# Optimization experiments

Hardware: AMD Instinct MI355X
Metric: run time of the kernel (lower is better)

The kernel has to match this reference:

```python
import jax, jax.numpy as jnp
import numpy as np

D_VOC, P_VOC, M_VOC = 2048, 1024, 4096
H = 256
T = 32
LD, LP, LM = 24, 12, 20


def _norm_adj(key, n):
    # binary graph + self loops, row-normalized (matches GCN.normalize(adj+I))
    a = (jax.random.uniform(key, (n, n)) < 0.002).astype(jnp.float32)
    a = a + jnp.eye(n, dtype=jnp.float32)
    rs = a.sum(axis=1)
    rinv = jnp.where(rs > 0, 1.0 / rs, 0.0)
    return rinv[:, None] * a


def setup_inputs() -> dict:
    key = jax.random.key(0)
    ks = jax.random.split(key, 32)
    s = float(1.0 / np.sqrt(H))
    u = lambda k, shape, sc: jax.random.uniform(k, shape, minval=-sc, maxval=sc, dtype=jnp.float32)
    inp = {
        'diag_codes': jax.random.randint(ks[0], (T, LD), 0, D_VOC),
        'proc_codes': jax.random.randint(ks[1], (T, LP), 0, P_VOC),
        'med_codes': jax.random.randint(ks[2], (T - 1, LM), 0, M_VOC),
        'diag_emb': u(ks[3], (D_VOC, H), 0.1),
        'proc_emb': u(ks[4], (P_VOC, H), 0.1),
        'gru_d_wih': u(ks[5], (3 * H, H), s), 'gru_d_whh': u(ks[6], (3 * H, H), s),
        'gru_d_bih': u(ks[7], (3 * H,), s), 'gru_d_bhh': u(ks[8], (3 * H,), s),
        'gru_p_wih': u(ks[9], (3 * H, H), s), 'gru_p_whh': u(ks[10], (3 * H, H), s),
        'gru_p_bih': u(ks[11], (3 * H,), s), 'gru_p_bhh': u(ks[12], (3 * H,), s),
        'q_w': u(ks[13], (2 * H, H), s), 'q_b': u(ks[14], (H,), s),
        'adj_ehr': _norm_adj(ks[15], M_VOC),
        'adj_ddi': _norm_adj(ks[16], M_VOC),
        'w1_ehr': u(ks[17], (M_VOC, H), s), 'b1_ehr': u(ks[18], (H,), s),
        'w2_ehr': u(ks[19], (H, H), s), 'b2_ehr': u(ks[20], (H,), s),
        'w1_ddi': u(ks[21], (M_VOC, H), s), 'b1_ddi': u(ks[22], (H,), s),
        'w2_ddi': u(ks[23], (H, H), s), 'b2_ddi': u(ks[24], (H,), s),
        'inter': jax.random.normal(ks[25], (1,), dtype=jnp.float32) / H,
        'proj_w': u(ks[26], (2 * H, H), s), 'proj_b': u(ks[27], (H,), s),
    }
    return inp


def _gru(x, wih, whh, bih, bhh):
    # torch.nn.GRU cell math; x: [T, H] -> outputs [T, H]
    def step(h, xt):
        gi = xt @ wih.T + bih
        gh = h @ whh.T + bhh
        ir, iz, inn = jnp.split(gi, 3)
        hr, hz, hn = jnp.split(gh, 3)
        r = jax.nn.sigmoid(ir + hr)
        z = jax.nn.sigmoid(iz + hz)
        n = jnp.tanh(inn + r * hn)
        h2 = (1.0 - z) * n + z * h
        return h2, h2
    _, ys = jax.lax.scan(step, jnp.zeros((x.shape[-1],), x.dtype), x)
    return ys


def _gcn(adj, w1, b1, w2, b2):
    # input features are identity, so first support mm(I, w1) == w1
    h1 = jax.nn.relu(adj @ w1 + b1)
    return adj @ (h1 @ w2) + b2


def reference(diag_codes, proc_codes, med_codes, diag_emb, proc_emb,
              gru_d_wih, gru_d_whh, gru_d_bih, gru_d_bhh,
              gru_p_wih, gru_p_whh, gru_p_bih, gru_p_bhh,
              q_w, q_b, adj_ehr, adj_ddi,
              w1_ehr, b1_ehr, w2_ehr, b2_ehr,
              w1_ddi, b1_ddi, w2_ddi, b2_ddi,
              inter, proj_w, proj_b):
    # ---- PatientEncoder: gather + sum codes per visit, GRU over visits ----
    seq_d = diag_emb[diag_codes].sum(axis=1)            # [T, H]
    seq_p = proc_emb[proc_codes].sum(axis=1)            # [T, H]
    od = _gru(seq_d, gru_d_wih, gru_d_whh, gru_d_bih, gru_d_bhh)
    op = _gru(seq_p, gru_p_wih, gru_p_whh, gru_p_bih, gru_p_bhh)
    feats = jnp.concatenate([od, op], axis=-1)          # [T, 2H]
    queries = jax.nn.relu(feats) @ q_w + q_b            # [T, H] (Sequential(ReLU, Linear))
    query = queries[-1:]                                # [1, H]
    history_keys = queries[:-1]                         # [T-1, H]
    # multi-hot history medication values (scatter)
    tm1 = med_codes.shape[0]
    history_values = jnp.zeros((tm1, M_VOC), jnp.float32).at[
        jnp.arange(tm1)[:, None], med_codes].set(1.0)   # [T-1, M_VOC]
    # ---- PriorEncoder ----
    prior = _gcn(adj_ehr, w1_ehr, b1_ehr, w2_ehr, b2_ehr) \
        - inter[0] * _gcn(adj_ddi, w1_ddi, b1_ddi, w2_ddi, b2_ddi)  # [M_VOC, H]
    w_emb = jax.nn.softmax(query @ prior.T, axis=-1)    # [1, M_VOC]
    # diag(w) @ prior == broadcast row-scale (the fused gather-weighted-scale)
    gc1 = w_emb.reshape(-1, 1) * prior                  # [M_VOC, H]
    visit_w = jax.nn.softmax(query @ history_keys.T, axis=-1)  # [1, T-1]
    wv = (visit_w @ history_values).reshape(-1, 1)      # [M_VOC, 1]
    gc2 = wv * prior                                    # [M_VOC, H]
    return jnp.concatenate([gc1, gc2], axis=-1) @ proj_w + proj_b  # [M_VOC, H]
```

## Files before the change

### kernel.cpp

```cpp
#include <hip/hip_runtime.h>
#include <hip/hip_bf16.h>

#define HD   256
#define TT   32
#define MV   4096
#define LD_  24
#define LP_  12
#define LM_  20
#define MAXNZ 96

typedef _Float16 h2v __attribute__((ext_vector_type(2)));
typedef _Float16 h8  __attribute__((ext_vector_type(8)));

__device__ __forceinline__ float fdot2(h2v a, h2v b, float c) {
#if __has_builtin(__builtin_amdgcn_fdot2)
  return __builtin_amdgcn_fdot2(a, b, c, false);
#else
  return c + (float)a[0] * (float)b[0] + (float)a[1] * (float)b[1];
#endif
}

#define PIN2(x) { float _t = __builtin_bit_cast(float, x); \
                  asm volatile("" : "+v"(_t));             \
                  x = __builtin_bit_cast(h2v, _t); }

__global__ __launch_bounds__(768) void k01_prep(
    const float* __restrict__ whh_d, const float* __restrict__ whh_p,
    h8* __restrict__ wt,
    const int* __restrict__ dc, const int* __restrict__ pc,
    const float* __restrict__ demb, const float* __restrict__ pemb,
    const float* __restrict__ wih_d, const float* __restrict__ bih_d,
    const float* __restrict__ wih_p, const float* __restrict__ bih_p,
    float* __restrict__ GI)
{
  if (blockIdx.y < 2) {
    const int i = blockIdx.x, b = blockIdx.y, g = threadIdx.x;
    const float* whh = b ? whh_p : whh_d;
    const float* src = whh + (size_t)g * HD + 8 * i;
    h8 v;
#pragma unroll
    for (int e = 0; e < 8; ++e) v[e] = (_Float16)src[e];
    wt[((size_t)b * 32 + i) * 768 + g] = v;
    return;
  }
  const int t = blockIdx.x, b = blockIdx.y - 2;
  const int* codes = b ? pc : dc;
  const int L = b ? LP_ : LD_;
  const float* emb = b ? pemb : demb;
  const float* wih = b ? wih_p : wih_d;
  const float* bih = b ? bih_p : bih_d;
  __shared__ float s[HD];
  const int j = threadIdx.x;
  if (j < HD) {
    float acc = 0.f;
    for (int l = 0; l < L; ++l) acc += emb[(size_t)codes[t * L + l] * HD + j];
    s[j] = acc;
  }
  __syncthreads();
  const int g = j;
  float acc = bih[g];
  const float* wr = wih + (size_t)g * HD;
  for (int k = 0; k < HD; k += 4) {
    float4 w4 = *(const float4*)(wr + k);
    acc = fmaf(w4.x, s[k], acc);
    acc = fmaf(w4.y, s[k + 1], acc);
    acc = fmaf(w4.z, s[k + 2], acc);
    acc = fmaf(w4.w, s[k + 3], acc);
  }
  GI[((size_t)b * TT + t) * 768 + g] = acc;
}

__global__ __launch_bounds__(512)
__attribute__((amdgpu_waves_per_eu(2, 2)))
void k2_gru(
    const float* __restrict__ GI, const h8* __restrict__ wt,
    const float* __restrict__ bhh_d, const float* __restrict__ bhh_p,
    float* __restrict__ feats)
{
  const int b = blockIdx.x, t = threadIdx.x;
  const int p = t >> 1;
  const int hk = t & 1;
  const float* gi = GI + (size_t)b * TT * 768;
  const float* bhh = b ? bhh_p : bhh_d;

  __shared__ h8 hbuf[2][32];

  h2v w[192];
  {
    const h8* wbase = wt + (size_t)b * 32 * 768;
#pragma unroll
    for (int r3 = 0; r3 < 3; ++r3) {
#pragma unroll
      for (int ii = 0; ii < 16; ++ii) {
        union { h8 v; h2v q[4]; } u;
        u.v = wbase[(size_t)(hk * 16 + ii) * 768 + r3 * 256 + p];
        w[(r3 * 16 + ii) * 4 + 0] = u.q[0];
        w[(r3 * 16 + ii) * 4 + 1] = u.q[1];
        w[(r3 * 16 + ii) * 4 + 2] = u.q[2];
        w[(r3 * 16 + ii) * 4 + 3] = u.q[3];
      }
    }
  }
#pragma unroll
  for (int i = 0; i < 192; ++i) PIN2(w[i])

  const float bh_r = bhh[p], bh_z = bhh[256 + p], bh_n = bhh[512 + p];
  float hreg = 0.f;
  if (t < 256) ((_Float16*)&hbuf[0][0])[t] = (_Float16)0.f;
  __syncthreads();

  for (int tt = 0; tt < TT; ++tt) {
    const float* git = gi + tt * 768;
    float ir = 0.f, iz = 0.f, inn = 0.f;
    if (hk == 0) { ir = git[p]; iz = git[256 + p]; inn = git[512 + p]; }

    const h8* hb = hbuf[tt & 1];
    float dr0 = 0.f, dr1 = 0.f, dz0 = 0.f, dz1 = 0.f, dn0 = 0.f, dn1 = 0.f;
#pragma unroll
    for (int ii = 0; ii < 16; ++ii) {
      union { h8 v; h2v q[4]; } u;
      u.v = hb[hk * 16 + ii];
      dr0 = fdot2(w[(0 * 16 + ii) * 4 + 0], u.q[0], dr0);
      dr1 = fdot2(w[(0 * 16 + ii) * 4 + 1], u.q[1], dr1);
      dr0 = fdot2(w[(0 * 16 + ii) * 4 + 2], u.q[2], dr0);
      dr1 = fdot2(w[(0 * 16 + ii) * 4 + 3], u.q[3], dr1);
      dz0 = fdot2(w[(1 * 16 + ii) * 4 + 0], u.q[0], dz0);
      dz1 = fdot2(w[(1 * 16 + ii) * 4 + 1], u.q[1], dz1);
      dz0 = fdot2(w[(1 * 16 + ii) * 4 + 2], u.q[2], dz0);
      dz1 = fdot2(w[(1 * 16 + ii) * 4 + 3], u.q[3], dz1);
      dn0 = fdot2(w[(2 * 16 + ii) * 4 + 0], u.q[0], dn0);
      dn1 = fdot2(w[(2 * 16 + ii) * 4 + 1], u.q[1], dn1);
      dn0 = fdot2(w[(2 * 16 + ii) * 4 + 2], u.q[2], dn0);
      dn1 = fdot2(w[(2 * 16 + ii) * 4 + 3], u.q[3], dn1);
    }
    float dr = dr0 + dr1, dz = dz0 + dz1, dn = dn0 + dn1;
    dr += __shfl_xor(dr, 1, 64);
    dz += __shfl_xor(dz, 1, 64);
    dn += __shfl_xor(dn, 1, 64);
    if (hk == 0) {
      const float hr = dr + bh_r, hz = dz + bh_z, hn = dn + bh_n;
      const float r = 1.f / (1.f + __expf(-(ir + hr)));
      const float z = 1.f / (1.f + __expf(-(iz + hz)));
      const float n = tanhf(inn + r * hn);
      hreg = (1.f - z) * n + z * hreg;
      ((_Float16*)&hbuf[(tt & 1) ^ 1][0])[p] = (_Float16)hreg;
      feats[(size_t)tt * 512 + b * HD + p] = hreg;
    }
    __syncthreads();
  }
}

#define LOADC(V0, V1, V2, V3, COFF)                               \
  V0 = *(const float4*)(adj + (COFF) + 0 * 256 + lane * 4);       \
  V1 = *(const float4*)(adj + (COFF) + 1 * 256 + lane * 4);       \
  V2 = *(const float4*)(adj + (COFF) + 2 * 256 + lane * 4);       \
  V3 = *(const float4*)(adj + (COFF) + 3 * 256 + lane * 4);

#define PROCC(V0, V1, V2, V3, COFF)                                     \
  {                                                                     \
    int cl = 0;                                                         \
    cl += (V0.x != 0.f) + (V0.y != 0.f) + (V0.z != 0.f) + (V0.w != 0.f);\
    cl += (V1.x != 0.f) + (V1.y != 0.f) + (V1.z != 0.f) + (V1.w != 0.f);\
    cl += (V2.x != 0.f) + (V2.y != 0.f) + (V2.z != 0.f) + (V2.w != 0.f);\
    cl += (V3.x != 0.f) + (V3.y != 0.f) + (V3.z != 0.f) + (V3.w != 0.f);\
    int pref = cl;                                                      \
    _Pragma("unroll")                                                   \
    for (int ofs = 1; ofs < 64; ofs <<= 1) {                            \
      int v = __shfl_up(pref, ofs, 64);                                 \
      if (lane >= ofs) pref += v;                                       \
    }                                                                   \
    const int ctotal = __shfl(pref, 63, 64);                            \
    int pos = base + pref - cl;                                         \
    const float4 vv4[4] = {V0, V1, V2, V3};                             \
    _Pragma("unroll")                                                   \
    for (int k = 0; k < 4; ++k) {                                       \
      const float vv[4] = {vv4[k].x, vv4[k].y, vv4[k].z, vv4[k].w};     \
      _Pragma("unroll")                                                 \
      for (int e = 0; e < 4; ++e) {                                     \
        if (vv[e] != 0.f) {                                             \
          if (pos < MAXNZ) { cg[pos] = (COFF) + k * 256 + lane * 4 + e; \
                             vg[pos] = vv[e]; }                         \
          ++pos;                                                        \
        }                                                               \
      }                                                                 \
    }                                                                   \
    base += ctotal;                                                     \
  }

__global__ __launch_bounds__(256) void k3_scan(
    const float* __restrict__ adj_e, const float* __restrict__ adj_d,
    int* __restrict__ cnt_g, int* __restrict__ cols_g,
    float* __restrict__ vals_g)
{
  const int w = threadIdx.x >> 6, lane = threadIdx.x & 63;
  const int rg = blockIdx.x * 4 + w;
  const int bsel = rg >> 12;
  const int r = rg & (MV - 1);
  const float* adj = (bsel ? adj_d : adj_e) + (size_t)r * MV;
  int* cg = cols_g + (size_t)rg * MAXNZ;
  float* vg = vals_g + (size_t)rg * MAXNZ;

  int base = 0;
  float4 a0, a1, a2, a3, b0, b1, b2, b3;
  LOADC(a0, a1, a2, a3, 0)
  LOADC(b0, b1, b2, b3, 1024)
  PROCC(a0, a1, a2, a3, 0)
  LOADC(a0, a1, a2, a3, 2048)
  PROCC(b0, b1, b2, b3, 1024)
  LOADC(b0, b1, b2, b3, 3072)
  PROCC(a0, a1, a2, a3, 2048)
  PROCC(b0, b1, b2, b3, 3072)

  if (lane == 0) cnt_g[rg] = base > MAXNZ ? MAXNZ : base;
}

__global__ __launch_bounds__(256) void k2b_queries(
    const float* __restrict__ feats, const float* __restrict__ q_w,
    const float* __restrict__ q_b, float* __restrict__ queries)
{
  const int t = blockIdx.x, j = threadIdx.x;
  __shared__ float f[512];
  f[j] = fmaxf(feats[(size_t)t * 512 + j], 0.f);
  f[j + 256] = fmaxf(feats[(size_t)t * 512 + 256 + j], 0.f);
  __syncthreads();
  float acc = q_b[j];
  for (int k = 0; k < 512; ++k) acc = fmaf(f[k], q_w[(size_t)k * HD + j], acc);
  queries[(size_t)t * HD + j] = acc;
}

__global__ __launch_bounds__(512) void k45_z(
    const int* __restrict__ cnt_g, const int* __restrict__ cols_g,
    const float* __restrict__ vals_g,
    const float* __restrict__ w1_e, const float* __restrict__ b1_e,
    const float* __restrict__ w1_d, const float* __restrict__ b1_d,
    const float* __restrict__ w2_e, const float* __restrict__ w2_d,
    float* __restrict__ zz)
{
  const int blk = blockIdx.x, b = blockIdx.y;
  const int t = threadIdx.x;
  __shared__ float tile[8][HD];
  __shared__ float part[8][HD];

  {
    const int w = t >> 6, lane = t & 63;
    const int rg = b * MV + blk * 8 + w;
    const float* w1 = b ? w1_d : w1_e;
    const float* b1 = b ? b1_d : b1_e;
    const int n = cnt_g[rg];
    const int* cg = cols_g + (size_t)rg * MAXNZ;
    const float* vg = vals_g + (size_t)rg * MAXNZ;
    float4 acc = *(const float4*)(b1 + lane * 4);
    for (int k = 0; k < n; ++k) {
      const int col = cg[k];
      const float v = vg[k];
      const float4 wv4 = *(const float4*)(w1 + (size_t)col * HD + lane * 4);
      acc.x = fmaf(v, wv4.x, acc.x);
      acc.y = fmaf(v, wv4.y, acc.y);
      acc.z = fmaf(v, wv4.z, acc.z);
      acc.w = fmaf(v, wv4.w, acc.w);
    }
    float4* dst = (float4*)&tile[w][lane * 4];
    dst->x = fmaxf(acc.x, 0.f); dst->y = fmaxf(acc.y, 0.f);
    dst->z = fmaxf(acc.z, 0.f); dst->w = fmaxf(acc.w, 0.f);
  }
  __syncthreads();

  const int j = t & 255, half = t >> 8;
  const float* w2 = b ? w2_d : w2_e;
  float acc[8];
#pragma unroll
  for (int r = 0; r < 8; ++r) acc[r] = 0.f;
  const int k0 = half * 128;
  for (int k = k0; k < k0 + 128; k += 4) {
    float wa = w2[(size_t)(k + 0) * HD + j];
    float wb = w2[(size_t)(k + 1) * HD + j];
    float wc = w2[(size_t)(k + 2) * HD + j];
    float wd = w2[(size_t)(k + 3) * HD + j];
#pragma unroll
    for (int r = 0; r < 8; ++r) {
      float4 tv = *(const float4*)&tile[r][k];
      acc[r] = fmaf(tv.x, wa, acc[r]);
      acc[r] = fmaf(tv.y, wb, acc[r]);
      acc[r] = fmaf(tv.z, wc, acc[r]);
      acc[r] = fmaf(tv.w, wd, acc[r]);
    }
  }
  if (half == 1) {
#pragma unroll
    for (int r = 0; r < 8; ++r) part[r][j] = acc[r];
  }
  __syncthreads();
  if (half == 0) {
    float* zb = zz + (size_t)b * MV * HD + (size_t)blk * 8 * HD;
#pragma unroll
    for (int r = 0; r < 8; ++r) zb[r * HD + j] = acc[r] + part[r][j];
  }
}

__global__ __launch_bounds__(256) void k5_prior(
    const float* __restrict__ zz, const int* __restrict__ cnt_g,
    const int* __restrict__ cols_g, const float* __restrict__ vals_g,
    const float* __restrict__ b2_e, const float* __restrict__ b2_d,
    const float* __restrict__ inter, const float* __restrict__ queries,
    float* __restrict__ prior, float* __restrict__ s1)
{
  const int r = blockIdx.x, j = threadIdx.x;
  __shared__ float red[256];
  float acc_e = b2_e[j];
  {
    const int ne = cnt_g[r];
    const int* ce = cols_g + (size_t)r * MAXNZ;
    const float* ve = vals_g + (size_t)r * MAXNZ;
    for (int k = 0; k < ne; ++k)
      acc_e = fmaf(ve[k], zz[(size_t)ce[k] * HD + j], acc_e);
  }
  float acc_d = b2_d[j];
  {
    const int nd = cnt_g[MV + r];
    const int* cd = cols_g + (size_t)(MV + r) * MAXNZ;
    const float* vd = vals_g + (size_t)(MV + r) * MAXNZ;
    const float* zd = zz + (size_t)MV * HD;
    for (int k = 0; k < nd; ++k)
      acc_d = fmaf(vd[k], zd[(size_t)cd[k] * HD + j], acc_d);
  }
  const float pr = acc_e - inter[0] * acc_d;
  prior[(size_t)r * HD + j] = pr;
  red[j] = queries[31 * HD + j] * pr;
  __syncthreads();
  for (int s = 128; s > 0; s >>= 1) {
    if (j < s) red[j] += red[j + s];
    __syncthreads();
  }
  if (j == 0) s1[r] = red[0];
}

__global__ __launch_bounds__(1024) void k6a_softmax(
    const float* __restrict__ s1, const float* __restrict__ queries,
    float* __restrict__ w_emb, float* __restrict__ visw)
{
  const int j = threadIdx.x;
  __shared__ float red[1024];
  __shared__ float s2[31];
  float m = -1e30f;
  for (int i = j; i < MV; i += 1024) m = fmaxf(m, s1[i]);
  red[j] = m;
  __syncthreads();
  for (int s = 512; s > 0; s >>= 1) {
    if (j < s) red[j] = fmaxf(red[j], red[j + s]);
    __syncthreads();
  }
  const float mx = red[0];
  __syncthreads();
  float sum = 0.f;
  for (int i = j; i < MV; i += 1024) sum += __expf(s1[i] - mx);
  red[j] = sum;
  __syncthreads();
  for (int s = 512; s > 0; s >>= 1) {
    if (j < s) red[j] += red[j + s];
    __syncthreads();
  }
  const float inv = 1.f / red[0];
  for (int i = j; i < MV; i += 1024) w_emb[i] = __expf(s1[i] - mx) * inv;

  if (j < 31) {
    float acc = 0.f;
    for (int k = 0; k < HD; ++k)
      acc = fmaf(queries[31 * HD + k], queries[(size_t)j * HD + k], acc);
    s2[j] = acc;
  }
  __syncthreads();
  if (j == 0) {
    float mm = -1e30f;
    for (int t = 0; t < 31; ++t) mm = fmaxf(mm, s2[t]);
    float ss = 0.f;
    for (int t = 0; t < 31; ++t) ss += __expf(s2[t] - mm);
    const float is = 1.f / ss;
    for (int t = 0; t < 31; ++t) visw[t] = __expf(s2[t] - mm) * is;
  }
}

__global__ __launch_bounds__(512) void k7_out(
    const float* __restrict__ prior, const float* __restrict__ w_emb,
    const float* __restrict__ visw, const int* __restrict__ med,
    const float* __restrict__ proj_w, const float* __restrict__ proj_b,
    float* __restrict__ out)
{
  const int blk = blockIdx.x;
  const int t = threadIdx.x;
  const int j = t & 255, half = t >> 8;
  const int r0 = blk * 8;
  __shared__ float tile[8][HD];
  __shared__ float part[8][HD];
  __shared__ float we[8], wvv[8];
  __shared__ int mc[31 * LM_];
  {
    float4* t4 = (float4*)tile;
    const float4* s4 = (const float4*)(prior + (size_t)r0 * HD);
    t4[t] = s4[t];
  }
  for (int i = t; i < 31 * LM_; i += 512) mc[i] = med[i];
  if (t < 8) we[t] = w_emb[r0 + t];
  __syncthreads();

  if (half == 0) {
    const int r = j >> 5, tp = j & 31;
    float contrib = 0.f;
    if (tp < 31) {
      const int m = r0 + r;
      bool found = false;
#pragma unroll
      for (int l = 0; l < LM_; ++l) found = found || (mc[tp * LM_ + l] == m);
      if (found) contrib = visw[tp];
    }
#pragma unroll
    for (int msk = 16; msk > 0; msk >>= 1) contrib += __shfl_xor(contrib, msk, 32);
    if (tp == 0) wvv[r] = contrib;
  }

  const float* wmat = proj_w + (size_t)half * HD * HD;
  float acc[8];
#pragma unroll
  for (int r = 0; r < 8; ++r) acc[r] = 0.f;
  for (int k = 0; k < HD; k += 4) {
    float wa = wmat[(size_t)(k + 0) * HD + j];
    float wb = wmat[(size_t)(k + 1) * HD + j];
    float wc = wmat[(size_t)(k + 2) * HD + j];
    float wd = wmat[(size_t)(k + 3) * HD + j];
#pragma unroll
    for (int r = 0; r < 8; ++r) {
      float4 tv = *(const float4*)&tile[r][k];
      acc[r] = fmaf(tv.x, wa, acc[r]);
      acc[r] = fmaf(tv.y, wb, acc[r]);
      acc[r] = fmaf(tv.z, wc, acc[r]);
      acc[r] = fmaf(tv.w, wd, acc[r]);
    }
  }
  if (half == 1) {
#pragma unroll
    for (int r = 0; r < 8; ++r) part[r][j] = acc[r];
  }
  __syncthreads();
  if (half == 0) {
    const float pb = proj_b[j];
#pragma unroll
    for (int r = 0; r < 8; ++r)
      out[(size_t)(r0 + r) * HD + j] = we[r] * acc[r] + wvv[r] * part[r][j] + pb;
  }
}

extern "C" void kernel_launch(void* const* d_in, const int* in_sizes, int n_in,
                              void* d_out, int out_size, void* d_ws, size_t ws_size,
                              hipStream_t stream) {
  const int* diag_codes = (const int*)d_in[0];
  const int* proc_codes = (const int*)d_in[1];
  const int* med_codes  = (const int*)d_in[2];
  const float* diag_emb = (const float*)d_in[3];
  const float* proc_emb = (const float*)d_in[4];
  const float* wih_d = (const float*)d_in[5];
  const float* whh_d = (const float*)d_in[6];
  const float* bih_d = (const float*)d_in[7];
  const float* bhh_d = (const float*)d_in[8];
  const float* wih_p = (const float*)d_in[9];
  const float* whh_p = (const float*)d_in[10];
  const float* bih_p = (const float*)d_in[11];
  const float* bhh_p = (const float*)d_in[12];
  const float* q_w = (const float*)d_in[13];
  const float* q_b = (const float*)d_in[14];
  const float* adj_ehr = (const float*)d_in[15];
  const float* adj_ddi = (const float*)d_in[16];
  const float* w1_ehr = (const float*)d_in[17];
  const float* b1_ehr = (const float*)d_in[18];
  const float* w2_ehr = (const float*)d_in[19];
  const float* b2_ehr = (const float*)d_in[20];
  const float* w1_ddi = (const float*)d_in[21];
  const float* b1_ddi = (const float*)d_in[22];
  const float* w2_ddi = (const float*)d_in[23];
  const float* b2_ddi = (const float*)d_in[24];
  const float* inter = (const float*)d_in[25];
  const float* proj_w = (const float*)d_in[26];
  const float* proj_b = (const float*)d_in[27];
  float* out = (float*)d_out;

  float* ws = (float*)d_ws;
  size_t off = 0;
  float* GI      = ws + off; off += 2 * TT * 768;
  float* feats   = ws + off; off += TT * 512;
  float* queries = ws + off; off += TT * HD;
  float* zz      = ws + off; off += 2 * (size_t)MV * HD;
  float* prior   = ws + off; off += (size_t)MV * HD;
  float* s1      = ws + off; off += MV;
  float* w_emb   = ws + off; off += MV;
  float* visw    = ws + off; off += 32;
  int*   cnt_g   = (int*)(ws + off); off += 2 * MV;
  int*   cols_g  = (int*)(ws + off); off += 2 * (size_t)MV * MAXNZ;
  float* vals_g  = ws + off; off += 2 * (size_t)MV * MAXNZ;
  h8*    wt      = (h8*)(ws + off); off += 2 * 32 * 768 * 4;
  (void)ws_size; (void)in_sizes; (void)n_in; (void)out_size;

  k01_prep<<<dim3(32, 4), 768, 0, stream>>>(whh_d, whh_p, wt,
      diag_codes, proc_codes, diag_emb, proc_emb,
      wih_d, bih_d, wih_p, bih_p, GI);
  k3_scan<<<2 * MV / 4, 256, 0, stream>>>(adj_ehr, adj_ddi,
      cnt_g, cols_g, vals_g);
  k2_gru<<<2, 512, 0, stream>>>(GI, wt, bhh_d, bhh_p, feats);
  k2b_queries<<<TT, 256, 0, stream>>>(feats, q_w, q_b, queries);
  k45_z<<<dim3(MV / 8, 2), 512, 0, stream>>>(cnt_g, cols_g, vals_g,
      w1_ehr, b1_ehr, w1_ddi, b1_ddi, w2_ehr, w2_ddi, zz);
  k5_prior<<<MV, 256, 0, stream>>>(zz, cnt_g, cols_g, vals_g, b2_ehr, b2_ddi,
      inter, queries, prior, s1);
  k6a_softmax<<<1, 1024, 0, stream>>>(s1, queries, w_emb, visw);
  k7_out<<<MV / 8, 512, 0, stream>>>(prior, w_emb, visw, med_codes,
      proj_w, proj_b, out);
}
```

Before: 208.2 us.

## Stream adjacency rows into LDS via global_load_lds in the sparse scan

The adjacency scan kernel now issues direct global-to-LDS loads (global_load_lds) for the whole 4096-float row of each wave, waits on them, then does the nonzero compaction by reading from LDS. The grid shrinks to 512 blocks, each wave looping over four rows. This is meant to put many more bytes in flight per wave and skip routing the row through VGPRs. The cost is a full vmcnt(0) wait before any compute with no overlap across rows, 64 KB of LDS per block that limits occupancy, and fewer blocks.

```diff
diff --git a/kernel.cpp b/kernel.cpp
--- a/kernel.cpp
+++ b/kernel.cpp
@@ -11,6 +11,9 @@
 
 typedef _Float16 h2v __attribute__((ext_vector_type(2)));
 typedef _Float16 h8  __attribute__((ext_vector_type(8)));
+
+typedef __attribute__((address_space(1))) const void* gas_t;
+typedef __attribute__((address_space(3))) void* las_t;
 
 __device__ __forceinline__ float fdot2(h2v a, h2v b, float c) {
 #if __has_builtin(__builtin_amdgcn_fdot2)
@@ -112,7 +115,7 @@
   for (int tt = 0; tt < TT; ++tt) {
     const float* git = gi + tt * 768;
     float ir = 0.f, iz = 0.f, inn = 0.f;
-    if (hk == 0) { ir = git[p]; iz = git[256 + p]; inn = git[512 + p]; }
+    if (hk == 0) { ir = git[p]; iz = git[256 + p]; inn = git[2 * 256 + p]; }
 
     const h8* hb = hbuf[tt & 1];
     float dr0 = 0.f, dr1 = 0.f, dz0 = 0.f, dz1 = 0.f, dn0 = 0.f, dn1 = 0.f;
@@ -150,68 +153,67 @@
   }
 }
 
-#define LOADC(V0, V1, V2, V3, COFF)                               \
-  V0 = *(const float4*)(adj + (COFF) + 0 * 256 + lane * 4);       \
-  V1 = *(const float4*)(adj + (COFF) + 1 * 256 + lane * 4);       \
-  V2 = *(const float4*)(adj + (COFF) + 2 * 256 + lane * 4);       \
-  V3 = *(const float4*)(adj + (COFF) + 3 * 256 + lane * 4);
-
-#define PROCC(V0, V1, V2, V3, COFF)                                     \
-  {                                                                     \
-    int cl = 0;                                                         \
-    cl += (V0.x != 0.f) + (V0.y != 0.f) + (V0.z != 0.f) + (V0.w != 0.f);\
-    cl += (V1.x != 0.f) + (V1.y != 0.f) + (V1.z != 0.f) + (V1.w != 0.f);\
-    cl += (V2.x != 0.f) + (V2.y != 0.f) + (V2.z != 0.f) + (V2.w != 0.f);\
-    cl += (V3.x != 0.f) + (V3.y != 0.f) + (V3.z != 0.f) + (V3.w != 0.f);\
-    int pref = cl;                                                      \
-    _Pragma("unroll")                                                   \
-    for (int ofs = 1; ofs < 64; ofs <<= 1) {                            \
-      int v = __shfl_up(pref, ofs, 64);                                 \
-      if (lane >= ofs) pref += v;                                       \
-    }                                                                   \
-    const int ctotal = __shfl(pref, 63, 64);                            \
-    int pos = base + pref - cl;                                         \
-    const float4 vv4[4] = {V0, V1, V2, V3};                             \
-    _Pragma("unroll")                                                   \
-    for (int k = 0; k < 4; ++k) {                                       \
-      const float vv[4] = {vv4[k].x, vv4[k].y, vv4[k].z, vv4[k].w};     \
-      _Pragma("unroll")                                                 \
-      for (int e = 0; e < 4; ++e) {                                     \
-        if (vv[e] != 0.f) {                                             \
-          if (pos < MAXNZ) { cg[pos] = (COFF) + k * 256 + lane * 4 + e; \
-                             vg[pos] = vv[e]; }                         \
-          ++pos;                                                        \
-        }                                                               \
-      }                                                                 \
-    }                                                                   \
-    base += ctotal;                                                     \
-  }
-
 __global__ __launch_bounds__(256) void k3_scan(
     const float* __restrict__ adj_e, const float* __restrict__ adj_d,
     int* __restrict__ cnt_g, int* __restrict__ cols_g,
     float* __restrict__ vals_g)
 {
+  __shared__ float buf[4][MV];
   const int w = threadIdx.x >> 6, lane = threadIdx.x & 63;
-  const int rg = blockIdx.x * 4 + w;
-  const int bsel = rg >> 12;
-  const int r = rg & (MV - 1);
-  const float* adj = (bsel ? adj_d : adj_e) + (size_t)r * MV;
-  int* cg = cols_g + (size_t)rg * MAXNZ;
-  float* vg = vals_g + (size_t)rg * MAXNZ;
-
-  int base = 0;
-  float4 a0, a1, a2, a3, b0, b1, b2, b3;
-  LOADC(a0, a1, a2, a3, 0)
-  LOADC(b0, b1, b2, b3, 1024)
-  PROCC(a0, a1, a2, a3, 0)
-  LOADC(a0, a1, a2, a3, 2048)
-  PROCC(b0, b1, b2, b3, 1024)
-  LOADC(b0, b1, b2, b3, 3072)
-  PROCC(a0, a1, a2, a3, 2048)
-  PROCC(b0, b1, b2, b3, 3072)
-
-  if (lane == 0) cnt_g[rg] = base > MAXNZ ? MAXNZ : base;
+  const int wg = blockIdx.x * 4 + w;
+
+  for (int it = 0; it < 4; ++it) {
+    const int rg = wg + it * 2048;
+    const int bsel = rg >> 12;
+    const int r = rg & (MV - 1);
+    const float* adj = (bsel ? adj_d : adj_e) + (size_t)r * MV;
+
+#pragma unroll
+    for (int c = 0; c < 16; ++c)
+      __builtin_amdgcn_global_load_lds(
+          (gas_t)(adj + c * 256 + lane * 4),
+          (las_t)(&buf[w][c * 256]), 16, 0, 0);
+    asm volatile("s_waitcnt vmcnt(0)" ::: "memory");
+
+    int base = 0;
+    int* cg = cols_g + (size_t)rg * MAXNZ;
+    float* vg = vals_g + (size_t)rg * MAXNZ;
+#pragma unroll
+    for (int c = 0; c < 4; ++c) {
+      const float4 v0 = *(const float4*)&buf[w][c * 1024 + 0 * 256 + lane * 4];
+      const float4 v1 = *(const float4*)&buf[w][c * 1024 + 1 * 256 + lane * 4];
+      const float4 v2 = *(const float4*)&buf[w][c * 1024 + 2 * 256 + lane * 4];
+      const float4 v3 = *(const float4*)&buf[w][c * 1024 + 3 * 256 + lane * 4];
+      int cl = 0;
+      cl += (v0.x != 0.f) + (v0.y != 0.f) + (v0.z != 0.f) + (v0.w != 0.f);
+      cl += (v1.x != 0.f) + (v1.y != 0.f) + (v1.z != 0.f) + (v1.w != 0.f);
+      cl += (v2.x != 0.f) + (v2.y != 0.f) + (v2.z != 0.f) + (v2.w != 0.f);
+      cl += (v3.x != 0.f) + (v3.y != 0.f) + (v3.z != 0.f) + (v3.w != 0.f);
+      int pref = cl;
+#pragma unroll
+      for (int ofs = 1; ofs < 64; ofs <<= 1) {
+        int v = __shfl_up(pref, ofs, 64);
+        if (lane >= ofs) pref += v;
+      }
+      const int ctot = __shfl(pref, 63, 64);
+      int pos = base + pref - cl;
+      const float4 vv4[4] = {v0, v1, v2, v3};
+#pragma unroll
+      for (int k = 0; k < 4; ++k) {
+        const float vv[4] = {vv4[k].x, vv4[k].y, vv4[k].z, vv4[k].w};
+#pragma unroll
+        for (int e = 0; e < 4; ++e) {
+          if (vv[e] != 0.f) {
+            if (pos < MAXNZ) { cg[pos] = c * 1024 + k * 256 + lane * 4 + e;
+                               vg[pos] = vv[e]; }
+            ++pos;
+          }
+        }
+      }
+      base += ctot;
+    }
+    if (lane == 0) cnt_g[rg] = base > MAXNZ ? MAXNZ : base;
+  }
 }
 
 __global__ __launch_bounds__(256) void k2b_queries(
@@ -500,7 +502,7 @@
   k01_prep<<<dim3(32, 4), 768, 0, stream>>>(whh_d, whh_p, wt,
       diag_codes, proc_codes, diag_emb, proc_emb,
       wih_d, bih_d, wih_p, bih_p, GI);
-  k3_scan<<<2 * MV / 4, 256, 0, stream>>>(adj_ehr, adj_ddi,
+  k3_scan<<<512, 256, 0, stream>>>(adj_ehr, adj_ddi,
       cnt_g, cols_g, vals_g);
   k2_gru<<<2, 512, 0, stream>>>(GI, wt, bhh_d, bhh_p, feats);
   k2b_queries<<<TT, 256, 0, stream>>>(feats, q_w, q_b, queries);
```

New measurement: 210.1 us. About the same (+0.9%).
